# Kernel optimization log

Measured on AMD Instinct MI355X. Metric: run time of the kernel, lower is better.

Reference implementation:

```python
import jax, jax.numpy as jnp
import numpy as np

H = 1024      # hidden_size
NH = 16       # num heads
HD = H // NH  # head dim


def setup_inputs() -> dict:
    key = jax.random.key(0)
    ks = jax.random.split(key, 10)
    s = 1.0 / np.sqrt(H)
    return {
        "hidden_states": jax.random.normal(ks[0], (2, 2048, H), jnp.float32),
        "attention_mask": jnp.zeros((2, 1, 1, 2048), jnp.float32),
        "Wq": jax.random.uniform(ks[1], (H, H), jnp.float32, -s, s),
        "bq": jnp.zeros((H,), jnp.float32),
        "Wk": jax.random.uniform(ks[2], (H, H), jnp.float32, -s, s),
        "bk": jnp.zeros((H,), jnp.float32),
        "Wv": jax.random.uniform(ks[3], (H, H), jnp.float32, -s, s),
        "bv": jnp.zeros((H,), jnp.float32),
        "Wo": jax.random.uniform(ks[4], (H, H), jnp.float32, -s, s),
        "bo": jnp.zeros((H,), jnp.float32),
    }


def _split_heads(x):
    b, s, _ = x.shape
    return x.reshape(b, s, NH, HD).transpose(0, 2, 1, 3)  # [B,NH,S,HD]


def reference(hidden_states, attention_mask, Wq, bq, Wk, bk, Wv, bv, Wo, bo):
    q = _split_heads(hidden_states @ Wq.T + bq)
    k = _split_heads(hidden_states @ Wk.T + bk)
    v = _split_heads(hidden_states @ Wv.T + bv)
    scores = jnp.einsum("bhqd,bhkd->bhqk", q, k) / np.sqrt(HD)
    scores = scores + attention_mask
    probs = jax.nn.softmax(scores, axis=-1)  # dropout prob=0 / eval mode -> no-op
    ctx = jnp.einsum("bhqk,bhkd->bhqd", probs, v)
    b, _, s, _ = ctx.shape
    ctx = ctx.transpose(0, 2, 1, 3).reshape(b, s, H)
    return ctx @ Wo.T + bo
```

## Files before the change

### kernel.cpp

```cpp
#include <hip/hip_runtime.h>
#include <hip/hip_bf16.h>

typedef __bf16 bf16_t;
typedef __bf16 bf16x8 __attribute__((ext_vector_type(8)));
typedef float f32x4 __attribute__((ext_vector_type(4)));
typedef float f32x16 __attribute__((ext_vector_type(16)));
typedef unsigned short u16;

#define DEVI __device__ __forceinline__
#define MFMA16x16x32(A, B, C) __builtin_amdgcn_mfma_f32_16x16x32_bf16(A, B, C, 0, 0, 0)
#define MFMA32x32x16(A, B, C) __builtin_amdgcn_mfma_f32_32x32x16_bf16(A, B, C, 0, 0, 0)

DEVI void gload_lds16(const void* g, void* l) {
  __builtin_amdgcn_global_load_lds(
      (const __attribute__((address_space(1))) void*)g,
      (__attribute__((address_space(3))) void*)l, 16, 0, 0);
}

DEVI u16 bits_of(bf16_t x) { return __builtin_bit_cast(u16, x); }

DEVI unsigned pk2(float lo, float hi) {
  return (unsigned)bits_of((bf16_t)lo) | ((unsigned)bits_of((bf16_t)hi) << 16);
}

DEVI bf16x8 mk_frag(unsigned s0, unsigned s1, unsigned s2, unsigned s3) {
  int4 t;
  t.x = (int)s0; t.y = (int)s1; t.z = (int)s2; t.w = (int)s3;
  return __builtin_bit_cast(bf16x8, t);
}

#if __has_builtin(__builtin_amdgcn_exp2f)
DEVI float exp2_fast(float x) { return __builtin_amdgcn_exp2f(x); }
#else
DEVI float exp2_fast(float x) { return __exp2f(x); }
#endif

__global__ void cvt_all(const float4* __restrict__ X,
                        const float4* __restrict__ Wq, const float4* __restrict__ Wk,
                        const float4* __restrict__ Wv, const float4* __restrict__ Wo,
                        ushort4* __restrict__ out) {
  int i = blockIdx.x * 256 + threadIdx.x;
  const float4* src;
  int off;
  if (i < 1048576) { src = X; off = i; }
  else {
    int j = i - 1048576;
    int seg = j >> 18;
    off = j & 262143;
    src = (seg == 0) ? Wq : (seg == 1) ? Wk : (seg == 2) ? Wv : Wo;
  }
  float4 v = src[off];
  ushort4 o;
  o.x = bits_of((bf16_t)v.x);
  o.y = bits_of((bf16_t)v.y);
  o.z = bits_of((bf16_t)v.z);
  o.w = bits_of((bf16_t)v.w);
  out[i] = o;
}

__global__ __launch_bounds__(256, 3) void gemm_bt(
    const bf16_t* __restrict__ A,
    const bf16_t* __restrict__ W0, const bf16_t* __restrict__ W1, const bf16_t* __restrict__ W2,
    const float* __restrict__ b0, const float* __restrict__ b1, const float* __restrict__ b2,
    bf16_t* o0, bf16_t* o1, bf16_t* o2, float s0, float s1, float s2) {
  constexpr int K = 1024, N = 1024;
  const int z = blockIdx.z;
  const bf16_t* W = (z == 0) ? W0 : ((z == 1) ? W1 : W2);
  const float* bias = (z == 0) ? b0 : ((z == 1) ? b1 : b2);
  bf16_t* out = (z == 0) ? o0 : ((z == 1) ? o1 : o2);
  const float scale = (z == 0) ? s0 : ((z == 1) ? s1 : s2);

  __shared__ bf16_t As[128 * 32];
  __shared__ bf16_t Bs[128 * 32];

  const int tid = threadIdx.x;
  const int wave = tid >> 6, lane = tid & 63;
  const int g = lane >> 4, l15 = lane & 15;
  const long m0 = (long)blockIdx.x * 128;
  const long n0 = (long)blockIdx.y * 128;

  const int srow = lane >> 2;
  const int scol = (lane & 3) * 8;

  const int wr = (wave >> 1) * 64;
  const int wc = (wave & 1) * 64;

  f32x4 acc[4][4] = {};

  for (int k0 = 0; k0 < K; k0 += 32) {
    __syncthreads();
#pragma unroll
    for (int t = 0; t < 2; ++t) {
      int chunk = wave * 2 + t;
      int row = chunk * 16 + srow;
      gload_lds16(A + (m0 + row) * K + k0 + scol, (char*)As + chunk * 1024);
      gload_lds16(W + (n0 + row) * K + k0 + scol, (char*)Bs + chunk * 1024);
    }
    __syncthreads();

    bf16x8 af[4], bfr[4];
#pragma unroll
    for (int i = 0; i < 4; ++i)
      af[i] = *(const bf16x8*)(As + (wr + i * 16 + l15) * 32 + g * 8);
#pragma unroll
    for (int i = 0; i < 4; ++i)
      bfr[i] = *(const bf16x8*)(Bs + (wc + i * 16 + l15) * 32 + g * 8);
    __builtin_amdgcn_s_setprio(1);
#pragma unroll
    for (int mi = 0; mi < 4; ++mi)
#pragma unroll
      for (int ni = 0; ni < 4; ++ni)
        acc[mi][ni] = MFMA16x16x32(af[mi], bfr[ni], acc[mi][ni]);
    __builtin_amdgcn_s_setprio(0);
  }

#pragma unroll
  for (int ni = 0; ni < 4; ++ni) {
    long col = n0 + wc + ni * 16 + l15;
    float bv = bias[col];
#pragma unroll
    for (int mi = 0; mi < 4; ++mi) {
#pragma unroll
      for (int r = 0; r < 4; ++r) {
        long row = m0 + wr + mi * 16 + g * 4 + r;
        out[row * N + col] = (bf16_t)((acc[mi][ni][r] + bv) * scale);
      }
    }
  }
}

__global__ __launch_bounds__(256, 3) void gemm_o64(
    const bf16_t* __restrict__ A, const bf16_t* __restrict__ W,
    const float* __restrict__ bias, float* __restrict__ out) {
  constexpr int K = 1024, N = 1024;
  __shared__ bf16_t As[128 * 32];
  __shared__ bf16_t Bs[64 * 32];

  const int tid = threadIdx.x;
  const int wave = tid >> 6, lane = tid & 63;
  const int g = lane >> 4, l15 = lane & 15;
  const long m0 = (long)blockIdx.x * 128;
  const long n0 = (long)blockIdx.y * 64;

  const int srow = lane >> 2;
  const int scol = (lane & 3) * 8;

  const int wr = (wave >> 1) * 64;
  const int wc = (wave & 1) * 32;

  f32x4 acc[4][2] = {};

  for (int k0 = 0; k0 < K; k0 += 32) {
    __syncthreads();
#pragma unroll
    for (int c = 0; c < 3; ++c) {
      int idx = wave * 3 + c;
      if (idx < 8) {
        int row = idx * 16 + srow;
        gload_lds16(A + (m0 + row) * K + k0 + scol, (char*)As + idx * 1024);
      } else {
        int row = (idx - 8) * 16 + srow;
        gload_lds16(W + (n0 + row) * K + k0 + scol, (char*)Bs + (idx - 8) * 1024);
      }
    }
    __syncthreads();

    bf16x8 af[4], bfr[2];
#pragma unroll
    for (int i = 0; i < 4; ++i)
      af[i] = *(const bf16x8*)(As + (wr + i * 16 + l15) * 32 + g * 8);
#pragma unroll
    for (int i = 0; i < 2; ++i)
      bfr[i] = *(const bf16x8*)(Bs + (wc + i * 16 + l15) * 32 + g * 8);
    __builtin_amdgcn_s_setprio(1);
#pragma unroll
    for (int mi = 0; mi < 4; ++mi)
#pragma unroll
      for (int ni = 0; ni < 2; ++ni)
        acc[mi][ni] = MFMA16x16x32(af[mi], bfr[ni], acc[mi][ni]);
    __builtin_amdgcn_s_setprio(0);
  }

#pragma unroll
  for (int ni = 0; ni < 2; ++ni) {
    long col = n0 + wc + ni * 16 + l15;
    float bv = bias[col];
#pragma unroll
    for (int mi = 0; mi < 4; ++mi) {
#pragma unroll
      for (int r = 0; r < 4; ++r) {
        long row = m0 + wr + mi * 16 + g * 4 + r;
        out[row * N + col] = acc[mi][ni][r] + bv;
      }
    }
  }
}

__global__ __launch_bounds__(128, 2) void attn_fwd5(
    const bf16_t* __restrict__ Qm, const bf16_t* __restrict__ Km,
    const bf16_t* __restrict__ Vm, const float* __restrict__ mask,
    bf16_t* __restrict__ ctx) {
  constexpr int S = 2048, Hs = 1024;
  constexpr float L2E = 1.4426950408889634f;
  int id = blockIdx.y * 32 + blockIdx.x;
  int swz = ((id & 7) << 7) | (id >> 3);
  const int qb = swz & 31;
  const int bh = swz >> 5;
  const int b = bh >> 4, h = bh & 15;

  const int tid = threadIdx.x;
  const int wave = tid >> 6, lane = tid & 63;
  const int l31 = lane & 31, hi = lane >> 5;

  __shared__ bf16_t Kb_[2][64 * 64];
  __shared__ bf16_t Vb_[2][64 * 64];
  __shared__ float Ms[2048];

  const char* Kg = (const char*)(Km + ((long)b * S) * Hs + h * 64);
  const bf16_t* Vg = Vm + ((long)b * S) * Hs + h * 64;
  const float* mrow = mask + b * S;

  const long qrow = (long)b * S + qb * 64 + wave * 32 + l31;
  const bf16_t* Qr = Qm + qrow * Hs + h * 64 + hi * 8;
  bf16x8 qB[4];
#pragma unroll
  for (int ks = 0; ks < 4; ++ks) qB[ks] = *(const bf16x8*)(Qr + ks * 16);

  const int ka = tid & 15, dq = tid >> 4;
  const bf16_t* Vsrc0 = Vg + (long)(4 * ka) * Hs + dq * 8;

  const int krow_in8 = lane >> 3;
  const int kslot = (lane & 7) ^ krow_in8;

#pragma unroll
  for (int c = 0; c < 4; ++c) {
    int ch = wave * 4 + c;
    gload_lds16((const char*)mrow + ch * 1024 + lane * 16, (char*)Ms + ch * 1024);
  }
#pragma unroll
  for (int c = 0; c < 4; ++c) {
    int ch = wave * 4 + c;
    gload_lds16(Kg + (long)(ch * 8 + krow_in8) * (Hs * 2) + kslot * 16,
                (char*)Kb_[0] + ch * 1024);
  }
  int4 v0 = *(const int4*)(Vsrc0);
  int4 v1 = *(const int4*)(Vsrc0 + Hs);
  int4 v2 = *(const int4*)(Vsrc0 + 2 * Hs);
  int4 v3 = *(const int4*)(Vsrc0 + 3 * Hs);
  {
    const u16* p0 = (const u16*)&v0; const u16* p1 = (const u16*)&v1;
    const u16* p2 = (const u16*)&v2; const u16* p3 = (const u16*)&v3;
#pragma unroll
    for (int j = 0; j < 8; ++j) {
      int d = dq * 8 + j;
      int2 w;
      w.x = (int)((unsigned)p0[j] | ((unsigned)p1[j] << 16));
      w.y = (int)((unsigned)p2[j] | ((unsigned)p3[j] << 16));
      *(int2*)((char*)Vb_[0] + d * 128 + ((8 * ka) ^ (j << 4))) = w;
    }
  }
  __syncthreads();

  f32x16 acc0 = {}, acc1 = {};
  float rho = 0.0f, lrun = 0.0f;
  bf16x8 pbP[4] = {};
  bf16x8 vaP[8] = {};

  for (int t = 0; t < 32; ++t) {
    const int cur = t & 1;
    const char* kb_c = (const char*)Kb_[cur];
    const char* vb_c = (const char*)Vb_[cur];

    bf16x8 kf0[4], kf1[4];
#pragma unroll
    for (int ks = 0; ks < 4; ++ks)
      kf0[ks] = *(const bf16x8*)(kb_c + l31 * 128 + (((2 * ks + hi) * 16) ^ ((l31 & 7) << 4)));
#pragma unroll
    for (int ks = 0; ks < 4; ++ks) {
      int row = 32 + l31;
      kf1[ks] = *(const bf16x8*)(kb_c + row * 128 + (((2 * ks + hi) * 16) ^ ((row & 7) << 4)));
    }

    if (t < 31) {
      const bf16_t* Vs = Vsrc0 + (long)((t + 1) * 64) * Hs;
      v0 = *(const int4*)(Vs);
      v1 = *(const int4*)(Vs + Hs);
      v2 = *(const int4*)(Vs + 2 * Hs);
      v3 = *(const int4*)(Vs + 3 * Hs);
#pragma unroll
      for (int c = 0; c < 4; ++c) {
        int ch = wave * 4 + c;
        gload_lds16(Kg + (long)((t + 1) * 64 + ch * 8 + krow_in8) * (Hs * 2) + kslot * 16,
                    (char*)Kb_[cur ^ 1] + ch * 1024);
      }
    }
    const float* mbase = Ms + t * 64;
    float4 mk[8];
#pragma unroll
    for (int st = 0; st < 2; ++st)
#pragma unroll
      for (int rg = 0; rg < 4; ++rg)
        mk[st * 4 + rg] = *(const float4*)(mbase + st * 32 + rg * 8 + hi * 4);

    f32x16 sc0 = {}, sc1 = {};
    __builtin_amdgcn_s_setprio(1);
#pragma unroll
    for (int ks = 0; ks < 4; ++ks) sc0 = MFMA32x32x16(kf0[ks], qB[ks], sc0);
#pragma unroll
    for (int ks = 0; ks < 4; ++ks) sc1 = MFMA32x32x16(kf1[ks], qB[ks], sc1);
    __builtin_amdgcn_s_setprio(0);

    if (t > 0) {
      __builtin_amdgcn_s_setprio(1);
#pragma unroll
      for (int st = 0; st < 2; ++st)
#pragma unroll
        for (int ks2 = 0; ks2 < 2; ++ks2) {
          int i = st * 2 + ks2;
          acc0 = MFMA32x32x16(vaP[i * 2 + 0], pbP[i], acc0);
          acc1 = MFMA32x32x16(vaP[i * 2 + 1], pbP[i], acc1);
        }
      __builtin_amdgcn_s_setprio(0);
    }

#pragma unroll
    for (int st = 0; st < 2; ++st)
#pragma unroll
      for (int ks2 = 0; ks2 < 2; ++ks2) {
        int slot = st * 4 + ks2 * 2 + hi;
        int i = st * 2 + ks2;
        vaP[i * 2 + 0] = *(const bf16x8*)(vb_c + l31 * 128 + ((slot * 16) ^ ((l31 & 7) << 4)));
        int d1 = 32 + l31;
        vaP[i * 2 + 1] = *(const bf16x8*)(vb_c + d1 * 128 + ((slot * 16) ^ ((d1 & 7) << 4)));
      }

    float m4[4] = {-1e30f, -1e30f, -1e30f, -1e30f};
#pragma unroll
    for (int st = 0; st < 2; ++st) {
      f32x16& s = st ? sc1 : sc0;
#pragma unroll
      for (int rg = 0; rg < 4; ++rg) {
        float4 m = mk[st * 4 + rg];
#pragma unroll
        for (int i = 0; i < 4; ++i) {
          float v = fmaf(((const float*)&m)[i], L2E, s[rg * 4 + i]);
          s[rg * 4 + i] = v;
          m4[i] = fmaxf(m4[i], v);
        }
      }
    }
    float mt = fmaxf(fmaxf(m4[0], m4[1]), fmaxf(m4[2], m4[3]));
    mt = fmaxf(mt, __shfl_xor(mt, 32, 64));

    if (!__all(mt - rho <= 24.0f)) {
      float mw = mt;
#pragma unroll
      for (int off = 1; off < 32; off <<= 1) mw = fmaxf(mw, __shfl_xor(mw, off, 64));
      float fct = exp2_fast(rho - mw);
      lrun *= fct;
#pragma unroll
      for (int i = 0; i < 16; ++i) { acc0[i] *= fct; acc1[i] *= fct; }
      rho = mw;
    }
    float rho_u = __builtin_amdgcn_readfirstlane(rho);
    if (rho_u != 0.0f) {
#pragma unroll
      for (int i = 0; i < 16; ++i) { sc0[i] -= rho_u; sc1[i] -= rho_u; }
    }

    float s4[4] = {0.f, 0.f, 0.f, 0.f};
#pragma unroll
    for (int st = 0; st < 2; ++st) {
      f32x16& s = st ? sc1 : sc0;
#pragma unroll
      for (int i = 0; i < 16; ++i) {
        float p = exp2_fast(s[i]);
        s[i] = p;
        s4[i & 3] += p;
      }
    }
    float ls = (s4[0] + s4[1]) + (s4[2] + s4[3]);
    ls += __shfl_xor(ls, 32, 64);
    lrun += ls;

#pragma unroll
    for (int st = 0; st < 2; ++st) {
      f32x16& s = st ? sc1 : sc0;
      unsigned a0 = pk2(s[0], s[1]),   b0 = pk2(s[4], s[5]);
      unsigned a1 = pk2(s[2], s[3]),   b1 = pk2(s[6], s[7]);
      unsigned a2 = pk2(s[8], s[9]),   b2 = pk2(s[12], s[13]);
      unsigned a3 = pk2(s[10], s[11]), b3 = pk2(s[14], s[15]);
      asm("v_permlane32_swap_b32 %0, %1" : "+v"(a0), "+v"(b0));
      asm("v_permlane32_swap_b32 %0, %1" : "+v"(a1), "+v"(b1));
      asm("v_permlane32_swap_b32 %0, %1" : "+v"(a2), "+v"(b2));
      asm("v_permlane32_swap_b32 %0, %1" : "+v"(a3), "+v"(b3));
      pbP[st * 2 + 0] = mk_frag(a0, a1, b0, b1);
      pbP[st * 2 + 1] = mk_frag(a2, a3, b2, b3);
    }

    if (t < 31) {
      const u16* p0 = (const u16*)&v0; const u16* p1 = (const u16*)&v1;
      const u16* p2 = (const u16*)&v2; const u16* p3 = (const u16*)&v3;
      char* vb_n = (char*)Vb_[cur ^ 1];
#pragma unroll
      for (int j = 0; j < 8; ++j) {
        int d = dq * 8 + j;
        int2 w;
        w.x = (int)((unsigned)p0[j] | ((unsigned)p1[j] << 16));
        w.y = (int)((unsigned)p2[j] | ((unsigned)p3[j] << 16));
        *(int2*)(vb_n + d * 128 + ((8 * ka) ^ (j << 4))) = w;
      }
    }
    __syncthreads();
  }

  __builtin_amdgcn_s_setprio(1);
#pragma unroll
  for (int st = 0; st < 2; ++st)
#pragma unroll
    for (int ks2 = 0; ks2 < 2; ++ks2) {
      int i = st * 2 + ks2;
      acc0 = MFMA32x32x16(vaP[i * 2 + 0], pbP[i], acc0);
      acc1 = MFMA32x32x16(vaP[i * 2 + 1], pbP[i], acc1);
    }
  __builtin_amdgcn_s_setprio(0);

  float inv = 1.0f / lrun;
  bf16_t* cb = ctx + qrow * Hs + h * 64;
#pragma unroll
  for (int dh = 0; dh < 2; ++dh) {
    f32x16& a = dh ? acc1 : acc0;
#pragma unroll
    for (int rg = 0; rg < 4; ++rg) {
      ushort4 o;
      o.x = bits_of((bf16_t)(a[rg * 4 + 0] * inv));
      o.y = bits_of((bf16_t)(a[rg * 4 + 1] * inv));
      o.z = bits_of((bf16_t)(a[rg * 4 + 2] * inv));
      o.w = bits_of((bf16_t)(a[rg * 4 + 3] * inv));
      *(ushort4*)(cb + dh * 32 + rg * 8 + hi * 4) = o;
    }
  }
}

extern "C" void kernel_launch(void* const* d_in, const int* in_sizes, int n_in,
                              void* d_out, int out_size, void* d_ws, size_t ws_size,
                              hipStream_t stream) {
  (void)in_sizes; (void)n_in; (void)out_size; (void)ws_size;
  const float* X  = (const float*)d_in[0];
  const float* mask = (const float*)d_in[1];
  const float* Wq = (const float*)d_in[2];
  const float* bq = (const float*)d_in[3];
  const float* Wk = (const float*)d_in[4];
  const float* bk = (const float*)d_in[5];
  const float* Wv = (const float*)d_in[6];
  const float* bv = (const float*)d_in[7];
  const float* Wo = (const float*)d_in[8];
  const float* bo = (const float*)d_in[9];

  char* ws = (char*)d_ws;
  bf16_t* Xb  = (bf16_t*)(ws + 0);
  bf16_t* Wqb = (bf16_t*)(ws + 8388608);
  bf16_t* Wkb = (bf16_t*)(ws + 10485760);
  bf16_t* Wvb = (bf16_t*)(ws + 12582912);
  bf16_t* Wob = (bf16_t*)(ws + 14680064);
  bf16_t* Qb  = (bf16_t*)(ws + 16777216);
  bf16_t* Kb  = (bf16_t*)(ws + 25165824);
  bf16_t* Vb  = (bf16_t*)(ws + 33554432);
  bf16_t* Cb  = (bf16_t*)(ws + 41943040);

  cvt_all<<<8192, 256, 0, stream>>>((const float4*)X, (const float4*)Wq, (const float4*)Wk,
                                    (const float4*)Wv, (const float4*)Wo, (ushort4*)Xb);

  const float QSCALE = 0.125f * 1.4426950408889634f;
  dim3 gq(32, 8, 3);
  gemm_bt<<<gq, 256, 0, stream>>>(Xb, Wqb, Wkb, Wvb, bq, bk, bv, Qb, Kb, Vb,
                                  QSCALE, 1.0f, 1.0f);

  dim3 ga(32, 32, 1);
  attn_fwd5<<<ga, 128, 0, stream>>>(Qb, Kb, Vb, mask, Cb);

  dim3 go(32, 16, 1);
  gemm_o64<<<go, 256, 0, stream>>>(Cb, Wob, bo, (float*)d_out);
}
```

Measured before the change: 127.8 us.

## Split attention KV sequence across two wave pairs and merge partial softmax results

The attention kernel grows from 128 to 256 threads. Two wave pairs each cover half of the key/value sequence for the same 64 query rows, and their partial outputs are merged through LDS with a log-sum-exp rescale. This halves the serial loop length per block and raises the number of waves in flight. In exchange it drops the K/V double buffering, so each pair reuses a single buffer with an extra barrier per iteration. It also adds an LDS reduction step at the end.

New measurement: 249.5 us. 1.95x slower.

```diff
diff --git a/kernel.cpp b/kernel.cpp
--- a/kernel.cpp
+++ b/kernel.cpp
@@ -196,7 +196,7 @@
   }
 }
 
-__global__ __launch_bounds__(128, 2) void attn_fwd5(
+__global__ __launch_bounds__(256, 4) void attn_fwd9(
     const bf16_t* __restrict__ Qm, const bf16_t* __restrict__ Km,
     const bf16_t* __restrict__ Vm, const float* __restrict__ mask,
     bf16_t* __restrict__ ctx) {
@@ -210,38 +210,36 @@
 
   const int tid = threadIdx.x;
   const int wave = tid >> 6, lane = tid & 63;
+  const int pair = wave >> 1;
+  const int waveq = wave & 1;
   const int l31 = lane & 31, hi = lane >> 5;
+  const int koff = pair * 1024;
 
   __shared__ bf16_t Kb_[2][64 * 64];
   __shared__ bf16_t Vb_[2][64 * 64];
   __shared__ float Ms[2048];
 
-  const char* Kg = (const char*)(Km + ((long)b * S) * Hs + h * 64);
-  const bf16_t* Vg = Vm + ((long)b * S) * Hs + h * 64;
+  const char* Kg = (const char*)(Km + ((long)b * S + koff) * Hs + h * 64);
+  const bf16_t* Vg = Vm + ((long)b * S + koff) * Hs + h * 64;
   const float* mrow = mask + b * S;
 
-  const long qrow = (long)b * S + qb * 64 + wave * 32 + l31;
+  const long qrow = (long)b * S + qb * 64 + waveq * 32 + l31;
   const bf16_t* Qr = Qm + qrow * Hs + h * 64 + hi * 8;
   bf16x8 qB[4];
 #pragma unroll
   for (int ks = 0; ks < 4; ++ks) qB[ks] = *(const bf16x8*)(Qr + ks * 16);
 
-  const int ka = tid & 15, dq = tid >> 4;
+  const int ptid = tid & 127;
+  const int ka = ptid & 15, dq = ptid >> 4;
   const bf16_t* Vsrc0 = Vg + (long)(4 * ka) * Hs + dq * 8;
 
   const int krow_in8 = lane >> 3;
   const int kslot = (lane & 7) ^ krow_in8;
 
 #pragma unroll
-  for (int c = 0; c < 4; ++c) {
-    int ch = wave * 4 + c;
+  for (int c = 0; c < 2; ++c) {
+    int ch = wave * 2 + c;
     gload_lds16((const char*)mrow + ch * 1024 + lane * 16, (char*)Ms + ch * 1024);
-  }
-#pragma unroll
-  for (int c = 0; c < 4; ++c) {
-    int ch = wave * 4 + c;
-    gload_lds16(Kg + (long)(ch * 8 + krow_in8) * (Hs * 2) + kslot * 16,
-                (char*)Kb_[0] + ch * 1024);
   }
   int4 v0 = *(const int4*)(Vsrc0);
   int4 v1 = *(const int4*)(Vsrc0 + Hs);
@@ -256,8 +254,14 @@
       int2 w;
       w.x = (int)((unsigned)p0[j] | ((unsigned)p1[j] << 16));
       w.y = (int)((unsigned)p2[j] | ((unsigned)p3[j] << 16));
-      *(int2*)((char*)Vb_[0] + d * 128 + ((8 * ka) ^ (j << 4))) = w;
-    }
+      *(int2*)((char*)Vb_[pair] + d * 128 + ((8 * ka) ^ (j << 4))) = w;
+    }
+  }
+#pragma unroll
+  for (int c = 0; c < 4; ++c) {
+    int ch = waveq * 4 + c;
+    gload_lds16(Kg + (long)(ch * 8 + krow_in8) * (Hs * 2) + kslot * 16,
+                (char*)Kb_[pair] + ch * 1024);
   }
   __syncthreads();
 
@@ -266,35 +270,29 @@
   bf16x8 pbP[4] = {};
   bf16x8 vaP[8] = {};
 
-  for (int t = 0; t < 32; ++t) {
-    const int cur = t & 1;
-    const char* kb_c = (const char*)Kb_[cur];
-    const char* vb_c = (const char*)Vb_[cur];
-
-    bf16x8 kf0[4], kf1[4];
-#pragma unroll
-    for (int ks = 0; ks < 4; ++ks)
-      kf0[ks] = *(const bf16x8*)(kb_c + l31 * 128 + (((2 * ks + hi) * 16) ^ ((l31 & 7) << 4)));
-#pragma unroll
-    for (int ks = 0; ks < 4; ++ks) {
-      int row = 32 + l31;
-      kf1[ks] = *(const bf16x8*)(kb_c + row * 128 + (((2 * ks + hi) * 16) ^ ((row & 7) << 4)));
-    }
-
-    if (t < 31) {
+  for (int t = 0; t < 16; ++t) {
+    const char* kb_c = (const char*)Kb_[pair];
+    const char* vb_c = (const char*)Vb_[pair];
+
+    if (t < 15) {
       const bf16_t* Vs = Vsrc0 + (long)((t + 1) * 64) * Hs;
       v0 = *(const int4*)(Vs);
       v1 = *(const int4*)(Vs + Hs);
       v2 = *(const int4*)(Vs + 2 * Hs);
       v3 = *(const int4*)(Vs + 3 * Hs);
-#pragma unroll
-      for (int c = 0; c < 4; ++c) {
-        int ch = wave * 4 + c;
-        gload_lds16(Kg + (long)((t + 1) * 64 + ch * 8 + krow_in8) * (Hs * 2) + kslot * 16,
-                    (char*)Kb_[cur ^ 1] + ch * 1024);
-      }
-    }
-    const float* mbase = Ms + t * 64;
+    }
+
+    bf16x8 kf0[4], kf1[4];
+#pragma unroll
+    for (int ks = 0; ks < 4; ++ks)
+      kf0[ks] = *(const bf16x8*)(kb_c + l31 * 128 + (((2 * ks + hi) * 16) ^ ((l31 & 7) << 4)));
+#pragma unroll
+    for (int ks = 0; ks < 4; ++ks) {
+      int row = 32 + l31;
+      kf1[ks] = *(const bf16x8*)(kb_c + row * 128 + (((2 * ks + hi) * 16) ^ ((row & 7) << 4)));
+    }
+
+    const float* mbase = Ms + pair * 1024 + t * 64;
     float4 mk[8];
 #pragma unroll
     for (int st = 0; st < 2; ++st)
@@ -313,13 +311,10 @@
     if (t > 0) {
       __builtin_amdgcn_s_setprio(1);
 #pragma unroll
-      for (int st = 0; st < 2; ++st)
-#pragma unroll
-        for (int ks2 = 0; ks2 < 2; ++ks2) {
-          int i = st * 2 + ks2;
-          acc0 = MFMA32x32x16(vaP[i * 2 + 0], pbP[i], acc0);
-          acc1 = MFMA32x32x16(vaP[i * 2 + 1], pbP[i], acc1);
-        }
+      for (int i5 = 0; i5 < 4; ++i5) {
+        acc0 = MFMA32x32x16(vaP[i5 * 2 + 0], pbP[i5], acc0);
+        acc1 = MFMA32x32x16(vaP[i5 * 2 + 1], pbP[i5], acc1);
+      }
       __builtin_amdgcn_s_setprio(0);
     }
 
@@ -328,10 +323,10 @@
 #pragma unroll
       for (int ks2 = 0; ks2 < 2; ++ks2) {
         int slot = st * 4 + ks2 * 2 + hi;
-        int i = st * 2 + ks2;
-        vaP[i * 2 + 0] = *(const bf16x8*)(vb_c + l31 * 128 + ((slot * 16) ^ ((l31 & 7) << 4)));
+        int i5 = st * 2 + ks2;
+        vaP[i5 * 2 + 0] = *(const bf16x8*)(vb_c + l31 * 128 + ((slot * 16) ^ ((l31 & 7) << 4)));
         int d1 = 32 + l31;
-        vaP[i * 2 + 1] = *(const bf16x8*)(vb_c + d1 * 128 + ((slot * 16) ^ ((d1 & 7) << 4)));
+        vaP[i5 * 2 + 1] = *(const bf16x8*)(vb_c + d1 * 128 + ((slot * 16) ^ ((d1 & 7) << 4)));
       }
 
     float m4[4] = {-1e30f, -1e30f, -1e30f, -1e30f};
@@ -386,58 +381,80 @@
 #pragma unroll
     for (int st = 0; st < 2; ++st) {
       f32x16& s = st ? sc1 : sc0;
-      unsigned a0 = pk2(s[0], s[1]),   b0 = pk2(s[4], s[5]);
-      unsigned a1 = pk2(s[2], s[3]),   b1 = pk2(s[6], s[7]);
-      unsigned a2 = pk2(s[8], s[9]),   b2 = pk2(s[12], s[13]);
-      unsigned a3 = pk2(s[10], s[11]), b3 = pk2(s[14], s[15]);
-      asm("v_permlane32_swap_b32 %0, %1" : "+v"(a0), "+v"(b0));
-      asm("v_permlane32_swap_b32 %0, %1" : "+v"(a1), "+v"(b1));
-      asm("v_permlane32_swap_b32 %0, %1" : "+v"(a2), "+v"(b2));
-      asm("v_permlane32_swap_b32 %0, %1" : "+v"(a3), "+v"(b3));
-      pbP[st * 2 + 0] = mk_frag(a0, a1, b0, b1);
-      pbP[st * 2 + 1] = mk_frag(a2, a3, b2, b3);
-    }
-
-    if (t < 31) {
+      unsigned a0 = pk2(s[0], s[1]),   c0 = pk2(s[4], s[5]);
+      unsigned a1 = pk2(s[2], s[3]),   c1 = pk2(s[6], s[7]);
+      unsigned a2 = pk2(s[8], s[9]),   c2 = pk2(s[12], s[13]);
+      unsigned a3 = pk2(s[10], s[11]), c3 = pk2(s[14], s[15]);
+      asm("v_permlane32_swap_b32 %0, %1" : "+v"(a0), "+v"(c0));
+      asm("v_permlane32_swap_b32 %0, %1" : "+v"(a1), "+v"(c1));
+      asm("v_permlane32_swap_b32 %0, %1" : "+v"(a2), "+v"(c2));
+      asm("v_permlane32_swap_b32 %0, %1" : "+v"(a3), "+v"(c3));
+      pbP[st * 2 + 0] = mk_frag(a0, a1, c0, c1);
+      pbP[st * 2 + 1] = mk_frag(a2, a3, c2, c3);
+    }
+    __syncthreads();
+
+    if (t < 15) {
       const u16* p0 = (const u16*)&v0; const u16* p1 = (const u16*)&v1;
       const u16* p2 = (const u16*)&v2; const u16* p3 = (const u16*)&v3;
-      char* vb_n = (char*)Vb_[cur ^ 1];
 #pragma unroll
       for (int j = 0; j < 8; ++j) {
         int d = dq * 8 + j;
         int2 w;
         w.x = (int)((unsigned)p0[j] | ((unsigned)p1[j] << 16));
         w.y = (int)((unsigned)p2[j] | ((unsigned)p3[j] << 16));
-        *(int2*)(vb_n + d * 128 + ((8 * ka) ^ (j << 4))) = w;
-      }
-    }
-    __syncthreads();
+        *(int2*)((char*)Vb_[pair] + d * 128 + ((8 * ka) ^ (j << 4))) = w;
+      }
+#pragma unroll
+      for (int c = 0; c < 4; ++c) {
+        int ch = waveq * 4 + c;
+        gload_lds16(Kg + (long)((t + 1) * 64 + ch * 8 + krow_in8) * (Hs * 2) + kslot * 16,
+                    (char*)Kb_[pair] + ch * 1024);
+      }
+      __syncthreads();
+    }
   }
 
   __builtin_amdgcn_s_setprio(1);
 #pragma unroll
-  for (int st = 0; st < 2; ++st)
-#pragma unroll
-    for (int ks2 = 0; ks2 < 2; ++ks2) {
-      int i = st * 2 + ks2;
-      acc0 = MFMA32x32x16(vaP[i * 2 + 0], pbP[i], acc0);
-      acc1 = MFMA32x32x16(vaP[i * 2 + 1], pbP[i], acc1);
-    }
+  for (int i5 = 0; i5 < 4; ++i5) {
+    acc0 = MFMA32x32x16(vaP[i5 * 2 + 0], pbP[i5], acc0);
+    acc1 = MFMA32x32x16(vaP[i5 * 2 + 1], pbP[i5], acc1);
+  }
   __builtin_amdgcn_s_setprio(0);
 
-  float inv = 1.0f / lrun;
-  bf16_t* cb = ctx + qrow * Hs + h * 64;
-#pragma unroll
-  for (int dh = 0; dh < 2; ++dh) {
-    f32x16& a = dh ? acc1 : acc0;
-#pragma unroll
-    for (int rg = 0; rg < 4; ++rg) {
-      ushort4 o;
-      o.x = bits_of((bf16_t)(a[rg * 4 + 0] * inv));
-      o.y = bits_of((bf16_t)(a[rg * 4 + 1] * inv));
-      o.z = bits_of((bf16_t)(a[rg * 4 + 2] * inv));
-      o.w = bits_of((bf16_t)(a[rg * 4 + 3] * inv));
-      *(ushort4*)(cb + dh * 32 + rg * 8 + hi * 4) = o;
+  float* accL = (float*)Kb_;
+  float2* lrL = (float2*)Ms;
+  if (pair == 1) {
+    float* dst = accL + waveq * 2048 + lane * 32;
+#pragma unroll
+    for (int i = 0; i < 16; ++i) dst[i] = acc0[i];
+#pragma unroll
+    for (int i = 0; i < 16; ++i) dst[16 + i] = acc1[i];
+    if (hi == 0) lrL[waveq * 32 + l31] = make_float2(lrun, rho);
+  }
+  __syncthreads();
+  if (pair == 0) {
+    const float* src = accL + waveq * 2048 + lane * 32;
+    float2 lrB = lrL[waveq * 32 + l31];
+    float M = fmaxf(rho, lrB.y);
+    float wA = exp2_fast(rho - M), wB = exp2_fast(lrB.y - M);
+    float inv = 1.0f / (lrun * wA + lrB.x * wB);
+    wA *= inv; wB *= inv;
+    bf16_t* cb = ctx + qrow * Hs + h * 64;
+#pragma unroll
+    for (int dh = 0; dh < 2; ++dh) {
+      f32x16& a = dh ? acc1 : acc0;
+      const float* sb = src + dh * 16;
+#pragma unroll
+      for (int rg = 0; rg < 4; ++rg) {
+        ushort4 o;
+        o.x = bits_of((bf16_t)(a[rg * 4 + 0] * wA + sb[rg * 4 + 0] * wB));
+        o.y = bits_of((bf16_t)(a[rg * 4 + 1] * wA + sb[rg * 4 + 1] * wB));
+        o.z = bits_of((bf16_t)(a[rg * 4 + 2] * wA + sb[rg * 4 + 2] * wB));
+        o.w = bits_of((bf16_t)(a[rg * 4 + 3] * wA + sb[rg * 4 + 3] * wB));
+        *(ushort4*)(cb + dh * 32 + rg * 8 + hi * 4) = o;
+      }
     }
   }
 }
@@ -477,7 +494,7 @@
                                   QSCALE, 1.0f, 1.0f);
 
   dim3 ga(32, 32, 1);
-  attn_fwd5<<<ga, 128, 0, stream>>>(Qb, Kb, Vb, mask, Cb);
+  attn_fwd9<<<ga, 256, 0, stream>>>(Qb, Kb, Vb, mask, Cb);
 
   dim3 go(32, 16, 1);
   gemm_o64<<<go, 256, 0, stream>>>(Cb, Wob, bo, (float*)d_out);
```
